# Performance work log

Hardware: AMD Instinct MI355X
Metric: run time of the kernel (lower is better)

## Reference

```python
import jax, jax.numpy as jnp
import numpy as np

B, T1, T2, D, H, NL, DFF, NC = 4, 128, 128, 512, 4, 4, 2048, 5
SQRT2 = 1.4142135623730951


def _ln(x, w, b, eps=1e-12):
    m = jnp.mean(x, -1, keepdims=True)
    v = jnp.mean((x - m) ** 2, -1, keepdims=True)
    return w * (x - m) / jnp.sqrt(v + eps) + b


def _gelu(x):  # erf-based gelu, as in source
    return x * 0.5 * (1.0 + jax.lax.erf(x / SQRT2))


def _mha(x, wq, bq, wk, bk, wv, bv, wo, bo):
    b, t, d = x.shape
    dk = d // H
    q = (x @ wq + bq).reshape(b, t, H, dk).transpose(0, 2, 1, 3)
    k = (x @ wk + bk).reshape(b, t, H, dk).transpose(0, 2, 1, 3)
    v = (x @ wv + bv).reshape(b, t, H, dk).transpose(0, 2, 1, 3)
    p = jax.nn.softmax(jnp.einsum('bhqd,bhkd->bhqk', q, k) / jnp.sqrt(jnp.float32(dk)), -1)
    o = jnp.einsum('bhqk,bhkd->bhqd', p, v).transpose(0, 2, 1, 3).reshape(b, t, d)
    return o @ wo + bo


def _encode(x, pos_emb, pe_w, pe_b, Wq, bq, Wk, bk, Wv, bv, Wo, bo,
            ff1_w, ff1_b, ff2_w, ff2_b, lnin_w, lnin_b, lnout_w, lnout_b):
    t = x.shape[1]
    x = _ln(x + pos_emb[:t], pe_w, pe_b)  # PositionalEncoding (dropout=0 eval)
    for i in range(Wq.shape[0]):  # EncoderLayer x NL
        x = x + _mha(x, Wq[i], bq[i], Wk[i], bk[i], Wv[i], bv[i], Wo[i], bo[i])
        h = _ln(x, lnin_w[i], lnin_b[i])
        x = x + (_gelu(h @ ff1_w[i] + ff1_b[i]) @ ff2_w[i] + ff2_b[i])
        x = _ln(x, lnout_w[i], lnout_b[i])
    return x


def _forward(q_emb, a_emb, qa_relation, aq_relation, concept_emb, pos_emb, pe_w, pe_b,
             Wq, bq, Wk, bk, Wv, bv, Wo, bo, ff1_w, ff1_b, ff2_w, ff2_b,
             lnin_w, lnin_b, lnout_w, lnout_b, sim_Wq, sim_bq, sim_Wk, sim_bk, cls_w, cls_b):
    enc = lambda x: _encode(x, pos_emb, pe_w, pe_b, Wq, bq, Wk, bk, Wv, bv, Wo, bo,
                            ff1_w, ff1_b, ff2_w, ff2_b, lnin_w, lnin_b, lnout_w, lnout_b)
    qe = enc(q_emb)   # [B,T1,D]
    ae = enc(a_emb)   # [B,T2,D]
    # ConceptEncoding: relation one-hots -> concept embedding mix
    hL = qa_relation @ concept_emb   # [B,T1,T2,D]
    hR = aq_relation @ concept_emb   # [B,T2,T1,D]
    # SimAttn: note source uses fwK for BOTH key and value, so v == k exactly
    q = qe @ sim_Wq + sim_bq
    k = ae @ sim_Wk + sim_bk
    kR = jnp.transpose(k[:, :, None, :] + hR, (0, 2, 1, 3))  # [B,T1,T2,D]
    scores = jnp.sum((q[:, :, None, :] + hL) * kR, axis=-1)   # [B,T1,T2]
    p = jax.nn.softmax(scores, -1)
    # sharpening branch (default sharpening=True): re-softmax the attention probs
    p = jnp.clip(jax.nn.softmax(1000.0 * p, -1), 0.0, 1.0)
    # value path: v + hR transposed == kR since v == k
    x = jnp.einsum('bts,btsd->btd', p, kR)                    # [B,T1,D]
    return jnp.mean(x, 1) @ cls_w + cls_b                     # [B,3]


def setup_inputs() -> dict:
    key = jax.random.key(0)
    rk = lambda i: jax.random.fold_in(key, i)
    w = lambda i, shape: 0.02 * jax.random.normal(rk(i), shape, jnp.float32)
    z = lambda shape: jnp.zeros(shape, jnp.float32)
    o = lambda shape: jnp.ones(shape, jnp.float32)
    return {
        'q_emb': jax.random.normal(rk(0), (B, T1, D), jnp.float32),
        'a_emb': jax.random.normal(rk(1), (B, T2, D), jnp.float32),
        'qa_relation': jax.random.uniform(rk(2), (B, T1, T2, NC), jnp.float32),
        'aq_relation': jax.random.uniform(rk(3), (B, T2, T1, NC), jnp.float32),
        'concept_emb': w(4, (NC, D)),
        'pos_emb': w(5, (512, D)),
        'pe_w': o((D,)), 'pe_b': z((D,)),
        'Wq': w(6, (NL, D, D)), 'bq': z((NL, D)),
        'Wk': w(7, (NL, D, D)), 'bk': z((NL, D)),
        'Wv': w(8, (NL, D, D)), 'bv': z((NL, D)),
        'Wo': w(9, (NL, D, D)), 'bo': z((NL, D)),
        'ff1_w': w(10, (NL, D, DFF)), 'ff1_b': z((NL, DFF)),
        'ff2_w': w(11, (NL, DFF, D)), 'ff2_b': z((NL, D)),
        'lnin_w': o((NL, D)), 'lnin_b': z((NL, D)),
        'lnout_w': o((NL, D)), 'lnout_b': z((NL, D)),
        'sim_Wq': w(12, (D, D)), 'sim_bq': z((D,)),
        'sim_Wk': w(13, (D, D)), 'sim_bk': z((D,)),
        'cls_w': w(14, (D, 3)), 'cls_b': z((3,)),
    }


def reference(q_emb, a_emb, qa_relation, aq_relation, concept_emb, pos_emb, pe_w, pe_b,
              Wq, bq, Wk, bk, Wv, bv, Wo, bo, ff1_w, ff1_b, ff2_w, ff2_b,
              lnin_w, lnin_b, lnout_w, lnout_b, sim_Wq, sim_bq, sim_Wk, sim_bk, cls_w, cls_b):
    return _forward(q_emb, a_emb, qa_relation, aq_relation, concept_emb, pos_emb, pe_w, pe_b,
                    Wq, bq, Wk, bk, Wv, bv, Wo, bo, ff1_w, ff1_b, ff2_w, ff2_b,
                    lnin_w, lnin_b, lnout_w, lnout_b, sim_Wq, sim_bq, sim_Wk, sim_bk, cls_w, cls_b)
```

## Files before the change

kernel.cpp:

```cpp
#include <hip/hip_runtime.h>
#include <hip/hip_bf16.h>
#include <math.h>

typedef unsigned short u16;
typedef __attribute__((ext_vector_type(8))) short bf16x8;
typedef __attribute__((ext_vector_type(4))) float f32x4;

__device__ __forceinline__ float ldin(const void* p, size_t i, int isbf) {
  if (isbf) return __bfloat162float(((const __hip_bfloat16*)p)[i]);
  return ((const float*)p)[i];
}
__device__ __forceinline__ float bfu(u16 u) { return __builtin_bit_cast(float, (unsigned)u << 16); }
__device__ __forceinline__ u16 f2bf(float x) {
  unsigned u = __builtin_bit_cast(unsigned, x);
  unsigned r = u + 0x7FFFu + ((u >> 16) & 1u);
  return (u16)(r >> 16);
}

__device__ __forceinline__ float wave_sum(float v) {
#pragma unroll
  for (int o = 32; o > 0; o >>= 1) v += __shfl_down(v, o);
  return v;
}

__device__ __forceinline__ float block_sum(float v, float* sbuf) {
  int lane = threadIdx.x & 63;
  int wid = threadIdx.x >> 6;
#pragma unroll
  for (int o = 32; o > 0; o >>= 1) v += __shfl_down(v, o);
  __syncthreads();
  if (lane == 0) sbuf[wid] = v;
  __syncthreads();
  int nw = blockDim.x >> 6;
  if (wid == 0) {
    float r = (lane < nw) ? sbuf[lane] : 0.f;
#pragma unroll
    for (int o = 4; o > 0; o >>= 1) r += __shfl_down(r, o);
    if (lane == 0) sbuf[0] = r;
  }
  __syncthreads();
  return sbuf[0];
}

__device__ __forceinline__ float block_max(float v, float* sbuf) {
  int lane = threadIdx.x & 63;
  int wid = threadIdx.x >> 6;
#pragma unroll
  for (int o = 32; o > 0; o >>= 1) v = fmaxf(v, __shfl_down(v, o));
  __syncthreads();
  if (lane == 0) sbuf[wid] = v;
  __syncthreads();
  int nw = blockDim.x >> 6;
  if (wid == 0) {
    float r = (lane < nw) ? sbuf[lane] : -INFINITY;
#pragma unroll
    for (int o = 4; o > 0; o >>= 1) r = fmaxf(r, __shfl_down(r, o));
    if (lane == 0) sbuf[0] = r;
  }
  __syncthreads();
  return sbuf[0];
}

__global__ void flag_kernel(const void* pe_w, int* flag) {
  if (threadIdx.x == 0 && blockIdx.x == 0)
    *flag = (((const unsigned short*)pe_w)[0] != 0) ? 1 : 0;
}

__global__ __launch_bounds__(256) void init_kernel(const void* pe_w, int* flag,
                                                   float* Sbuf, float* pabar) {
  int i = blockIdx.x * 256 + threadIdx.x;
  ((float4*)Sbuf)[i] = make_float4(0.f, 0.f, 0.f, 0.f);
  if (blockIdx.x == 0) {
    if (threadIdx.x == 0) *flag = (((const unsigned short*)pe_w)[0] != 0) ? 1 : 0;
    if (threadIdx.x < 20) pabar[threadIdx.x] = 0.f;
  }
}


__global__ __launch_bounds__(256) void convT2(
    const void* __restrict__ S0, const void* __restrict__ S1,
    const void* __restrict__ S2, const void* __restrict__ S3,
    size_t srcStride, int K, int N, u16* __restrict__ Dh, u16* __restrict__ Dl,
    size_t layerStride, size_t tensorStride, int tmask, int lshift,
    const int* __restrict__ dflag) {
  const int isbf = *dflag;
  int z = blockIdx.z;
  int t = z & tmask, l = z >> lshift;
  const void* S = (t == 0) ? S0 : ((t == 1) ? S1 : ((t == 2) ? S2 : S3));
  size_t soff = (size_t)l * srcStride;
  size_t doff = (size_t)l * layerStride + (size_t)t * tensorStride;
  int n0 = blockIdx.x * 32, k0 = blockIdx.y * 32;
  __shared__ float tt[32][33];
  int tx = threadIdx.x & 31, ty = threadIdx.x >> 5;
#pragma unroll
  for (int j = 0; j < 4; ++j) {
    int r = ty + j * 8;
    tt[r][tx] = ldin(S, soff + (size_t)(k0 + r) * N + n0 + tx, isbf);
  }
  __syncthreads();
#pragma unroll
  for (int j = 0; j < 4; ++j) {
    int r = ty + j * 8;
    float v = tt[tx][r];
    u16 h = f2bf(v);
    u16 lo = f2bf(v - bfu(h));
    size_t o = doff + (size_t)(n0 + r) * K + k0 + tx;
    Dh[o] = h;
    Dl[o] = lo;
  }
}

__global__ __launch_bounds__(256) void gemm_hl(
    const u16* __restrict__ Ahp, const u16* __restrict__ Alp, int lda,
    const u16* __restrict__ Whp, const u16* __restrict__ Wlp, int ldw,
    const void* __restrict__ b0, const void* __restrict__ b1, const void* __restrict__ b2,
    size_t bo0, size_t bo1, size_t bo2, int bshift,
    float* __restrict__ C, u16* __restrict__ Chp, u16* __restrict__ Clp,
    u16* __restrict__ Vh, u16* __restrict__ Vl, int ldc,
    int K, int act, int mode, int ysplit, size_t wrowoff1,
    const int* __restrict__ dflag) {
  const int isbf = *dflag;
  __shared__ __align__(16) u16 sAh[64][72];
  __shared__ __align__(16) u16 sAl[64][72];
  __shared__ __align__(16) u16 sBh[64][72];
  __shared__ __align__(16) u16 sBl[64][72];

  int tid = threadIdx.x;
  int by = blockIdx.y;
  int row0 = by * 64, col0 = blockIdx.x * 64;
  int rsplit = (by >= ysplit);
  size_t wrow0 = (size_t)col0 + (rsplit ? wrowoff1 : 0);
  if (mode == 5) wrow0 = wrowoff1 + (size_t)(by >> 1) * 128 + col0;
  int Ksub = K / (int)gridDim.z;
  int kstart = (int)blockIdx.z * Ksub;
  int addbias = (blockIdx.z == 0) && (mode != 5);

  int wid = tid >> 6, lane = tid & 63, quad = lane >> 4, lm = lane & 15;
  int mrow = (wid & 1) * 32, ncol = (wid >> 1) * 32;

  f32x4 acc[2][2] = {};

  int sr = tid >> 2, sc = (tid & 3) * 16;

  for (int k0 = kstart; k0 < kstart + Ksub; k0 += 64) {
    const u16* p;
    p = Ahp + (size_t)(row0 + sr) * lda + k0 + sc;
    uint4 a0 = *(const uint4*)p, a1 = *(const uint4*)(p + 8);
    p = Alp + (size_t)(row0 + sr) * lda + k0 + sc;
    uint4 a2 = *(const uint4*)p, a3 = *(const uint4*)(p + 8);
    p = Whp + (wrow0 + sr) * (size_t)ldw + k0 + sc;
    uint4 w0 = *(const uint4*)p, w1 = *(const uint4*)(p + 8);
    p = Wlp + (wrow0 + sr) * (size_t)ldw + k0 + sc;
    uint4 w2 = *(const uint4*)p, w3 = *(const uint4*)(p + 8);
    __syncthreads();
    *(uint4*)&sAh[sr][sc] = a0; *(uint4*)&sAh[sr][sc + 8] = a1;
    *(uint4*)&sAl[sr][sc] = a2; *(uint4*)&sAl[sr][sc + 8] = a3;
    *(uint4*)&sBh[sr][sc] = w0; *(uint4*)&sBh[sr][sc + 8] = w1;
    *(uint4*)&sBl[sr][sc] = w2; *(uint4*)&sBl[sr][sc + 8] = w3;
    __syncthreads();
#pragma unroll
    for (int ks = 0; ks < 2; ++ks) {
      bf16x8 ah[2], al[2], wh[2], wl[2];
#pragma unroll
      for (int mi = 0; mi < 2; ++mi) {
        ah[mi] = *(const bf16x8*)&sAh[mrow + mi * 16 + lm][ks * 32 + quad * 8];
        al[mi] = *(const bf16x8*)&sAl[mrow + mi * 16 + lm][ks * 32 + quad * 8];
      }
#pragma unroll
      for (int ni = 0; ni < 2; ++ni) {
        wh[ni] = *(const bf16x8*)&sBh[ncol + ni * 16 + lm][ks * 32 + quad * 8];
        wl[ni] = *(const bf16x8*)&sBl[ncol + ni * 16 + lm][ks * 32 + quad * 8];
      }
#pragma unroll
      for (int mi = 0; mi < 2; ++mi)
#pragma unroll
        for (int ni = 0; ni < 2; ++ni) {
          acc[mi][ni] = __builtin_amdgcn_mfma_f32_16x16x32_bf16(ah[mi], wh[ni], acc[mi][ni], 0, 0, 0);
          acc[mi][ni] = __builtin_amdgcn_mfma_f32_16x16x32_bf16(al[mi], wh[ni], acc[mi][ni], 0, 0, 0);
          acc[mi][ni] = __builtin_amdgcn_mfma_f32_16x16x32_bf16(ah[mi], wl[ni], acc[mi][ni], 0, 0, 0);
        }
    }
  }
#pragma unroll
  for (int mi = 0; mi < 2; ++mi) {
#pragma unroll
    for (int ni = 0; ni < 2; ++ni) {
      int colg = col0 + ncol + ni * 16 + lm;
      float bv = 0.f;
      if (addbias) {
        const void* bp; size_t bo;
        if (rsplit) { bp = b1; bo = bo1 + colg; }
        else {
          int seg = colg >> bshift;
          bp = (seg == 0) ? b0 : ((seg == 1) ? b1 : b2);
          bo = (seg == 0) ? bo0 : ((seg == 1) ? bo1 : bo2);
          bo += (size_t)colg - ((size_t)seg << bshift);
        }
        bv = ldin(bp, bo, isbf);
      }
#pragma unroll
      for (int r = 0; r < 4; ++r) {
        int rowg = row0 + mrow + mi * 16 + quad * 4 + r;
        float v = acc[mi][ni][r] + bv;
        if (act) v = v * 0.5f * (1.f + erff(v * 0.70710678118654752f));
        if (mode == 3 && colg >= 1024) {
          int gg = rowg >> 7;
          size_t o = ((size_t)(gg * 512) + (colg - 1024)) * 128 + (rowg & 127);
          u16 hh = f2bf(v); Vh[o] = hh; Vl[o] = f2bf(v - bfu(hh));
        } else {
          size_t o = (size_t)rowg * ldc + colg;
          if (mode == 0) C[o] = v;
          else if (mode == 1 || mode == 5) atomicAdd(&C[o], v);
          else if (mode == 4) {
            C[o] = v;
            u16 hh = f2bf(v); Chp[o] = hh; Clp[o] = f2bf(v - bfu(hh));
          } else {
            u16 hh = f2bf(v); Chp[o] = hh; Clp[o] = f2bf(v - bfu(hh));
          }
        }
      }
    }
  }
}

__global__ __launch_bounds__(256) void attn_mfma(
    const u16* __restrict__ Qh, const u16* __restrict__ Ql,
    const u16* __restrict__ Vth, const u16* __restrict__ Vtl,
    u16* __restrict__ Oh, u16* __restrict__ Ol) {
  int tq = blockIdx.x & 3;
  int h = (blockIdx.x >> 2) & 3;
  int g = blockIdx.x >> 4;
  int tid = threadIdx.x;
  int w = tid >> 6, lane = tid & 63, quad = lane >> 4, lm = lane & 15;
  __shared__ float S[32][132];

  f32x4 sacc[2][2] = {};
#pragma unroll
  for (int ks = 0; ks < 4; ++ks) {
    bf16x8 qh[2], ql[2];
#pragma unroll
    for (int mi = 0; mi < 2; ++mi) {
      size_t qi = (size_t)(g * 128 + tq * 32 + mi * 16 + lm) * 1536 + h * 128 + ks * 32 + quad * 8;
      qh[mi] = *(const bf16x8*)(Qh + qi);
      ql[mi] = *(const bf16x8*)(Ql + qi);
    }
#pragma unroll
    for (int ni = 0; ni < 2; ++ni) {
      size_t kix = (size_t)(g * 128 + w * 32 + ni * 16 + lm) * 1536 + 512 + h * 128 + ks * 32 + quad * 8;
      bf16x8 kh = *(const bf16x8*)(Qh + kix);
      bf16x8 kl = *(const bf16x8*)(Ql + kix);
#pragma unroll
      for (int mi = 0; mi < 2; ++mi) {
        sacc[mi][ni] = __builtin_amdgcn_mfma_f32_16x16x32_bf16(qh[mi], kh, sacc[mi][ni], 0, 0, 0);
        sacc[mi][ni] = __builtin_amdgcn_mfma_f32_16x16x32_bf16(ql[mi], kh, sacc[mi][ni], 0, 0, 0);
        sacc[mi][ni] = __builtin_amdgcn_mfma_f32_16x16x32_bf16(qh[mi], kl, sacc[mi][ni], 0, 0, 0);
      }
    }
  }
  const float scale = 0.08838834764831845f;
#pragma unroll
  for (int mi = 0; mi < 2; ++mi)
#pragma unroll
    for (int ni = 0; ni < 2; ++ni)
#pragma unroll
      for (int r = 0; r < 4; ++r)
        S[mi * 16 + quad * 4 + r][w * 32 + ni * 16 + lm] = sacc[mi][ni][r] * scale;
  __syncthreads();

  {
    int row = tid >> 3, j = tid & 7;
    float* sp = &S[row][j * 16];
    float v[16];
    *(float4*)(v) = *(float4*)(sp);
    *(float4*)(v + 4) = *(float4*)(sp + 4);
    *(float4*)(v + 8) = *(float4*)(sp + 8);
    *(float4*)(v + 12) = *(float4*)(sp + 12);
    float mx = v[0];
#pragma unroll
    for (int i = 1; i < 16; ++i) mx = fmaxf(mx, v[i]);
    mx = fmaxf(mx, __shfl_xor(mx, 1));
    mx = fmaxf(mx, __shfl_xor(mx, 2));
    mx = fmaxf(mx, __shfl_xor(mx, 4));
    float sum = 0.f;
#pragma unroll
    for (int i = 0; i < 16; ++i) { v[i] = expf(v[i] - mx); sum += v[i]; }
    sum += __shfl_xor(sum, 1);
    sum += __shfl_xor(sum, 2);
    sum += __shfl_xor(sum, 4);
    float inv = 1.f / sum;
#pragma unroll
    for (int i = 0; i < 16; ++i) v[i] *= inv;
    *(float4*)(sp) = *(float4*)(v);
    *(float4*)(sp + 4) = *(float4*)(v + 4);
    *(float4*)(sp + 8) = *(float4*)(v + 8);
    *(float4*)(sp + 12) = *(float4*)(v + 12);
  }
  __syncthreads();

  f32x4 oacc[2][2] = {};
#pragma unroll
  for (int ks = 0; ks < 4; ++ks) {
    bf16x8 ph[2], pl[2];
#pragma unroll
    for (int mi = 0; mi < 2; ++mi) {
      float pv[8];
      const float* srow = &S[mi * 16 + lm][ks * 32 + quad * 8];
      *(float4*)(pv) = *(const float4*)srow;
      *(float4*)(pv + 4) = *(const float4*)(srow + 4);
      bf16x8 hh, ll;
#pragma unroll
      for (int i = 0; i < 8; ++i) {
        u16 hb = f2bf(pv[i]);
        hh[i] = (short)hb;
        ll[i] = (short)f2bf(pv[i] - bfu(hb));
      }
      ph[mi] = hh; pl[mi] = ll;
    }
#pragma unroll
    for (int ni = 0; ni < 2; ++ni) {
      size_t vi = (size_t)(g * 512 + h * 128 + w * 32 + ni * 16 + lm) * 128 + ks * 32 + quad * 8;
      bf16x8 vh = *(const bf16x8*)(Vth + vi);
      bf16x8 vl = *(const bf16x8*)(Vtl + vi);
#pragma unroll
      for (int mi = 0; mi < 2; ++mi) {
        oacc[mi][ni] = __builtin_amdgcn_mfma_f32_16x16x32_bf16(ph[mi], vh, oacc[mi][ni], 0, 0, 0);
        oacc[mi][ni] = __builtin_amdgcn_mfma_f32_16x16x32_bf16(pl[mi], vh, oacc[mi][ni], 0, 0, 0);
        oacc[mi][ni] = __builtin_amdgcn_mfma_f32_16x16x32_bf16(ph[mi], vl, oacc[mi][ni], 0, 0, 0);
      }
    }
  }
#pragma unroll
  for (int mi = 0; mi < 2; ++mi)
#pragma unroll
    for (int ni = 0; ni < 2; ++ni)
#pragma unroll
      for (int r = 0; r < 4; ++r) {
        int t = tq * 32 + mi * 16 + quad * 4 + r;
        int d = w * 32 + ni * 16 + lm;
        size_t o = (size_t)(g * 128 + t) * 512 + h * 128 + d;
        float val = oacc[mi][ni][r];
        u16 hb = f2bf(val);
        Oh[o] = hb;
        Ol[o] = f2bf(val - bfu(hb));
      }
}

__global__ __launch_bounds__(256) void emb_ln2(
    const void* __restrict__ qe, const void* __restrict__ ae, const void* __restrict__ pos,
    const void* __restrict__ w, const void* __restrict__ b,
    float* __restrict__ x, u16* __restrict__ oh, u16* __restrict__ ol,
    const int* __restrict__ dflag) {
  const int isbf = *dflag;
  const int D = 512;
  int row = blockIdx.x;
  const void* emb = (row < 512) ? qe : ae;
  int lr = row & 511, t = row & 127;
  __shared__ float sbuf[8];
  int i0 = threadIdx.x, i1 = threadIdx.x + 256;
  float v0 = ldin(emb, (size_t)lr * D + i0, isbf) + ldin(pos, (size_t)t * D + i0, isbf);
  float v1 = ldin(emb, (size_t)lr * D + i1, isbf) + ldin(pos, (size_t)t * D + i1, isbf);
  float mean = block_sum(v0 + v1, sbuf) / 512.f;
  float d0 = v0 - mean, d1 = v1 - mean;
  float var = block_sum(d0 * d0 + d1 * d1, sbuf) / 512.f;
  float inv = 1.0f / sqrtf(var + 1e-12f);
  float r0 = ldin(w, i0, isbf) * d0 * inv + ldin(b, i0, isbf);
  float r1 = ldin(w, i1, isbf) * d1 * inv + ldin(b, i1, isbf);
  size_t o0 = (size_t)row * D + i0, o1 = (size_t)row * D + i1;
  x[o0] = r0; x[o1] = r1;
  u16 h0 = f2bf(r0); oh[o0] = h0; ol[o0] = f2bf(r0 - bfu(h0));
  u16 h1 = f2bf(r1); oh[o1] = h1; ol[o1] = f2bf(r1 - bfu(h1));
}

__global__ __launch_bounds__(256) void ln2(
    const float* __restrict__ in, float* __restrict__ outf,
    u16* __restrict__ oh, u16* __restrict__ ol,
    const void* __restrict__ w, const void* __restrict__ b, size_t wboff,
    const int* __restrict__ dflag) {
  const int isbf = *dflag;
  const int D = 512;
  int row = blockIdx.x;
  __shared__ float sbuf[8];
  int i0 = threadIdx.x, i1 = threadIdx.x + 256;
  float v0 = in[(size_t)row * D + i0];
  float v1 = in[(size_t)row * D + i1];
  float mean = block_sum(v0 + v1, sbuf) / 512.f;
  float d0 = v0 - mean, d1 = v1 - mean;
  float var = block_sum(d0 * d0 + d1 * d1, sbuf) / 512.f;
  float inv = 1.0f / sqrtf(var + 1e-12f);
  float r0 = ldin(w, wboff + i0, isbf) * d0 * inv + ldin(b, wboff + i0, isbf);
  float r1 = ldin(w, wboff + i1, isbf) * d1 * inv + ldin(b, wboff + i1, isbf);
  size_t o0 = (size_t)row * D + i0, o1 = (size_t)row * D + i1;
  if (outf) { outf[o0] = r0; outf[o1] = r1; }
  u16 h0 = f2bf(r0); oh[o0] = h0; ol[o0] = f2bf(r0 - bfu(h0));
  u16 h1 = f2bf(r1); oh[o1] = h1; ol[o1] = f2bf(r1 - bfu(h1));
}

__global__ __launch_bounds__(64) void projgram(const float* __restrict__ qkb,
                                               const void* __restrict__ ce,
                                               float* __restrict__ ck, float* __restrict__ G,
                                               const int* __restrict__ dflag) {
  const int isbf = *dflag;
  if (blockIdx.x < 1024) {
    int row = blockIdx.x;
#pragma unroll
    for (int c = 0; c < 5; ++c) {
      float acc = 0.f;
      for (int d = threadIdx.x; d < 512; d += 64)
        acc = fmaf(qkb[(size_t)row * 512 + d], ldin(ce, (size_t)c * 512 + d, isbf), acc);
      acc = wave_sum(acc);
      if (threadIdx.x == 0) ck[row * 5 + c] = acc;
    }
  } else {
    int i = blockIdx.x - 1024;
    int c = i / 5, c2 = i % 5;
    float acc = 0.f;
    for (int d = threadIdx.x; d < 512; d += 64)
      acc = fmaf(ldin(ce, (size_t)c * 512 + d, isbf), ldin(ce, (size_t)c2 * 512 + d, isbf), acc);
    acc = wave_sum(acc);
    if (threadIdx.x == 0) G[i] = acc;
  }
}

__global__ __launch_bounds__(256) void prep_rel(
    const void* __restrict__ aq, const void* __restrict__ qa,
    const float* __restrict__ ck, const float* __restrict__ G,
    float* __restrict__ R, const int* __restrict__ dflag) {
  const int isbf = *dflag;
  int bx = blockIdx.x;
  int t0 = (bx & 3) * 32;
  int s0 = ((bx >> 2) & 3) * 32;
  int b = bx >> 4;
  int tid = threadIdx.x;
  __shared__ float aqs[32][164];
  __shared__ float Gs[25];
  __shared__ float kcs[32][5];
  __shared__ float qcs[32][5];
  for (int i = tid; i < 5120; i += 256) {
    int s = i / 160, r = i % 160;
    aqs[s][r] = ldin(aq, ((size_t)(b * 128 + s0 + s) * 128 + t0) * 5 + r, isbf);
  }
  if (tid < 25) Gs[tid] = G[tid];
  for (int i = tid; i < 160; i += 256)
    kcs[i / 5][i % 5] = ck[(size_t)(512 + b * 128 + s0 + i / 5) * 5 + i % 5];
  for (int i = tid; i < 160; i += 256)
    qcs[i / 5][i % 5] = ck[(size_t)(b * 128 + t0 + i / 5) * 5 + i % 5];
  __syncthreads();
  for (int i = tid; i < 1024; i += 256) {
    int t = i >> 5, s = i & 31;
    size_t qoff = ((size_t)(b * 128 + t0 + t) * 128 + s0 + s) * 5;
    float r = 0.f;
#pragma unroll
    for (int c = 0; c < 5; ++c) {
      float ga = 0.f;
#pragma unroll
      for (int c2 = 0; c2 < 5; ++c2) ga = fmaf(Gs[c * 5 + c2], aqs[s][t * 5 + c2], ga);
      r = fmaf(ldin(qa, qoff + c, isbf), kcs[s][c] + ga, r);
      r = fmaf(aqs[s][t * 5 + c], qcs[t][c], r);
    }
    R[(size_t)(b * 128 + t0 + t) * 128 + s0 + s] = r;
  }
}

__global__ __launch_bounds__(128) void softmax_rel(
    const float* __restrict__ Sbuf, const float* __restrict__ R,
    float* __restrict__ PT) {
  int row = blockIdx.x;
  int b = row >> 7, t = row & 127;
  int s = threadIdx.x;
  __shared__ float sbuf[8];
  size_t o = (size_t)row * 128 + s;
  float sc = Sbuf[o] + R[o];
  float mx = block_max(sc, sbuf);
  float e = expf(sc - mx);
  float ssum = block_sum(e, sbuf);
  float p = e / ssum;
  float mx2 = block_max(p, sbuf);
  float e2 = expf(1000.f * (p - mx2));
  float s2 = block_sum(e2, sbuf);
  float pf = fminf(fmaxf(e2 / s2, 0.f), 1.f);
  PT[(size_t)(b * 128 + s) * 128 + t] = pf;
}

__global__ __launch_bounds__(64) void pbar2(
    const float* __restrict__ PT, const void* __restrict__ aq,
    float* __restrict__ Pbar, float* __restrict__ pabar,
    const int* __restrict__ dflag) {
  const int isbf = *dflag;
  int bs = blockIdx.x;
  int b = bs >> 7;
  int lane = threadIdx.x;
  int t0 = lane * 2;
  float2 pt = *(const float2*)(PT + (size_t)bs * 128 + t0);
  size_t ao = ((size_t)bs * 128 + t0) * 5;
  float psum = pt.x + pt.y;
  float pac[5];
#pragma unroll
  for (int c = 0; c < 5; ++c)
    pac[c] = pt.x * ldin(aq, ao + c, isbf) + pt.y * ldin(aq, ao + 5 + c, isbf);
  psum = wave_sum(psum);
#pragma unroll
  for (int c = 0; c < 5; ++c) pac[c] = wave_sum(pac[c]);
  if (lane == 0) {
    Pbar[bs] = psum;
#pragma unroll
    for (int c = 0; c < 5; ++c) atomicAdd(&pabar[b * 5 + c], pac[c]);
  }
}

__global__ __launch_bounds__(512) void meancls(
    const float* __restrict__ qkb, const float* __restrict__ Pbar, const float* __restrict__ pabar,
    const void* __restrict__ ce, const void* __restrict__ clsw, const void* __restrict__ clsb,
    void* __restrict__ out, const int* __restrict__ dflag) {
  const int isbf = *dflag;
  int b = blockIdx.x;
  int tid = threadIdx.x;
  __shared__ float Ps[128];
  __shared__ float pas[5];
  __shared__ float xm[512];
  __shared__ float sbuf[8];
  if (tid < 128) Ps[tid] = Pbar[b * 128 + tid];
  if (tid < 5) pas[tid] = pabar[b * 5 + tid];
  __syncthreads();
  int d = tid;
  const float* k = qkb + (size_t)(512 + b * 128) * 512 + d;
  float acc = 0.f;
  for (int s = 0; s < 128; ++s) acc = fmaf(Ps[s], k[(size_t)s * 512], acc);
#pragma unroll
  for (int c = 0; c < 5; ++c) acc = fmaf(pas[c], ldin(ce, (size_t)c * 512 + d, isbf), acc);
  acc *= (1.f / 128.f);
  xm[d] = acc;
  __syncthreads();
  for (int j = 0; j < 3; ++j) {
    float v = block_sum(xm[d] * ldin(clsw, (size_t)d * 3 + j, isbf), sbuf);
    if (d == 0) {
      float val = v + ldin(clsb, j, isbf);
      if (isbf) ((u16*)out)[b * 3 + j] = f2bf(val);
      else ((float*)out)[b * 3 + j] = val;
    }
    __syncthreads();
  }
}


__global__ __launch_bounds__(256) void gemm_mfma(
    const float* __restrict__ A, const void* __restrict__ W, size_t woff,
    const void* __restrict__ bias, size_t boff,
    float* __restrict__ C, int M, int N, int K, int act, int addto,
    const int* __restrict__ dflag) {
  const int isbf = *dflag;
  __shared__ __align__(16) u16 Ah[64][40];
  __shared__ __align__(16) u16 Al[64][40];
  __shared__ __align__(16) u16 Wh[64][40];
  __shared__ __align__(16) u16 Wl[64][40];
  int tid = threadIdx.x;
  int row0 = blockIdx.y * 64, col0 = blockIdx.x * 64;
  int wid = tid >> 6, lane = tid & 63;
  int quad = lane >> 4, lm = lane & 15;
  int mrow = (wid & 1) * 32, ncol = (wid >> 1) * 32;
  f32x4 acc[2][2] = {};
  int ar = tid >> 2, akc = (tid & 3) * 8;
  int bk = tid >> 3, bn0 = (tid & 7) * 8;
  for (int k0 = 0; k0 < K; k0 += 32) {
    const float* ap = A + (size_t)(row0 + ar) * K + k0 + akc;
    float av[8];
    *(float4*)(av) = *(const float4*)ap;
    *(float4*)(av + 4) = *(const float4*)(ap + 4);
    unsigned hp[4], lp[4];
#pragma unroll
    for (int j = 0; j < 4; ++j) {
      u16 h0 = f2bf(av[2 * j]);
      u16 h1 = f2bf(av[2 * j + 1]);
      u16 l0 = f2bf(av[2 * j] - bfu(h0));
      u16 l1 = f2bf(av[2 * j + 1] - bfu(h1));
      hp[j] = (unsigned)h0 | ((unsigned)h1 << 16);
      lp[j] = (unsigned)l0 | ((unsigned)l1 << 16);
    }
    *(uint4*)&Ah[ar][akc] = make_uint4(hp[0], hp[1], hp[2], hp[3]);
    *(uint4*)&Al[ar][akc] = make_uint4(lp[0], lp[1], lp[2], lp[3]);
    float wv[8];
    size_t welem = woff + (size_t)(k0 + bk) * N + col0 + bn0;
    if (isbf) {
      const u16* wp = (const u16*)W + welem;
      uint4 raw = *(const uint4*)wp;
      wv[0] = bfu((u16)(raw.x & 0xFFFF)); wv[1] = bfu((u16)(raw.x >> 16));
      wv[2] = bfu((u16)(raw.y & 0xFFFF)); wv[3] = bfu((u16)(raw.y >> 16));
      wv[4] = bfu((u16)(raw.z & 0xFFFF)); wv[5] = bfu((u16)(raw.z >> 16));
      wv[6] = bfu((u16)(raw.w & 0xFFFF)); wv[7] = bfu((u16)(raw.w >> 16));
    } else {
      const float* wp = (const float*)W + welem;
      *(float4*)(wv) = *(const float4*)wp;
      *(float4*)(wv + 4) = *(const float4*)(wp + 4);
    }
#pragma unroll
    for (int i = 0; i < 8; ++i) {
      u16 h = f2bf(wv[i]);
      u16 l = f2bf(wv[i] - bfu(h));
      Wh[bn0 + i][bk] = h;
      Wl[bn0 + i][bk] = l;
    }
    __syncthreads();
#pragma unroll
    for (int mi = 0; mi < 2; ++mi) {
      bf16x8 ah = *(const bf16x8*)&Ah[mrow + mi * 16 + lm][quad * 8];
      bf16x8 al = *(const bf16x8*)&Al[mrow + mi * 16 + lm][quad * 8];
#pragma unroll
      for (int ni = 0; ni < 2; ++ni) {
        bf16x8 wh = *(const bf16x8*)&Wh[ncol + ni * 16 + lm][quad * 8];
        bf16x8 wl = *(const bf16x8*)&Wl[ncol + ni * 16 + lm][quad * 8];
        acc[mi][ni] = __builtin_amdgcn_mfma_f32_16x16x32_bf16(ah, wh, acc[mi][ni], 0, 0, 0);
        acc[mi][ni] = __builtin_amdgcn_mfma_f32_16x16x32_bf16(al, wh, acc[mi][ni], 0, 0, 0);
        acc[mi][ni] = __builtin_amdgcn_mfma_f32_16x16x32_bf16(ah, wl, acc[mi][ni], 0, 0, 0);
      }
    }
    __syncthreads();
  }
#pragma unroll
  for (int mi = 0; mi < 2; ++mi) {
#pragma unroll
    for (int ni = 0; ni < 2; ++ni) {
      int colg = col0 + ncol + ni * 16 + lm;
      float bv = ldin(bias, boff + colg, isbf);
#pragma unroll
      for (int r = 0; r < 4; ++r) {
        int rowg = row0 + mrow + mi * 16 + quad * 4 + r;
        float v = acc[mi][ni][r] + bv;
        if (act) v = v * 0.5f * (1.f + erff(v * 0.70710678118654752f));
        size_t o = (size_t)rowg * N + colg;
        if (addto) C[o] += v; else C[o] = v;
      }
    }
  }
}

__global__ __launch_bounds__(256) void emb_ln_kernel(const void* __restrict__ emb,
                                                     const void* __restrict__ pos,
                                                     const void* __restrict__ w,
                                                     const void* __restrict__ b,
                                                     float* __restrict__ out, int T, int D,
                                                     const int* __restrict__ dflag) {
  const int isbf = *dflag;
  int row = blockIdx.x;
  int t = row % T;
  __shared__ float sbuf[8];
  int i0 = threadIdx.x, i1 = threadIdx.x + 256;
  float v0 = ldin(emb, (size_t)row * D + i0, isbf) + ldin(pos, (size_t)t * D + i0, isbf);
  float v1 = ldin(emb, (size_t)row * D + i1, isbf) + ldin(pos, (size_t)t * D + i1, isbf);
  float mean = block_sum(v0 + v1, sbuf) / (float)D;
  float d0 = v0 - mean, d1 = v1 - mean;
  float var = block_sum(d0 * d0 + d1 * d1, sbuf) / (float)D;
  float inv = 1.0f / sqrtf(var + 1e-12f);
  out[(size_t)row * D + i0] = ldin(w, i0, isbf) * d0 * inv + ldin(b, i0, isbf);
  out[(size_t)row * D + i1] = ldin(w, i1, isbf) * d1 * inv + ldin(b, i1, isbf);
}

__global__ __launch_bounds__(256) void ln_kernel(const float* __restrict__ in, float* __restrict__ out,
                                                 const void* __restrict__ w, const void* __restrict__ b,
                                                 size_t wboff, int D, const int* __restrict__ dflag) {
  const int isbf = *dflag;
  int row = blockIdx.x;
  __shared__ float sbuf[8];
  int i0 = threadIdx.x, i1 = threadIdx.x + 256;
  float v0 = in[(size_t)row * D + i0];
  float v1 = in[(size_t)row * D + i1];
  float mean = block_sum(v0 + v1, sbuf) / (float)D;
  float d0 = v0 - mean, d1 = v1 - mean;
  float var = block_sum(d0 * d0 + d1 * d1, sbuf) / (float)D;
  float inv = 1.0f / sqrtf(var + 1e-12f);
  out[(size_t)row * D + i0] = ldin(w, wboff + i0, isbf) * d0 * inv + ldin(b, wboff + i0, isbf);
  out[(size_t)row * D + i1] = ldin(w, wboff + i1, isbf) * d1 * inv + ldin(b, wboff + i1, isbf);
}

__global__ __launch_bounds__(128) void attn_kernel(const float* __restrict__ q, const float* __restrict__ k,
                                                   const float* __restrict__ v, float* __restrict__ o,
                                                   int B, int H, int T, int dk) {
  int t = blockIdx.x % T;
  int h = (blockIdx.x / T) % H;
  int b = blockIdx.x / (T * H);
  int D = H * dk;
  int tid = threadIdx.x;
  __shared__ float qs[128];
  __shared__ float ps[128];
  __shared__ float sbuf[8];
  qs[tid] = q[(size_t)(b * T + t) * D + h * dk + tid];
  __syncthreads();
  const float* krow = k + (size_t)(b * T + tid) * D + h * dk;
  float sc = 0.f;
#pragma unroll 8
  for (int d = 0; d < 128; ++d) sc = fmaf(qs[d], krow[d], sc);
  sc *= 0.08838834764831845f;
  float mx = block_max(sc, sbuf);
  float e = expf(sc - mx);
  float s = block_sum(e, sbuf);
  ps[tid] = e / s;
  __syncthreads();
  float acc = 0.f;
  for (int s2 = 0; s2 < 128; ++s2)
    acc = fmaf(ps[s2], v[(size_t)(b * T + s2) * D + h * dk + tid], acc);
  o[(size_t)(b * T + t) * D + h * dk + tid] = acc;
}

__global__ __launch_bounds__(64) void proj_ce_kernel(const float* __restrict__ q,
                                                     const void* __restrict__ ce,
                                                     float* __restrict__ out, int D, int NC,
                                                     const int* __restrict__ dflag) {
  const int isbf = *dflag;
  int row = blockIdx.x;
  for (int c = 0; c < NC; ++c) {
    float acc = 0.f;
    for (int d = threadIdx.x; d < D; d += 64)
      acc = fmaf(q[(size_t)row * D + d], ldin(ce, (size_t)c * D + d, isbf), acc);
    acc = wave_sum(acc);
    if (threadIdx.x == 0) out[row * NC + c] = acc;
  }
}

__global__ __launch_bounds__(64) void gram_kernel(const void* __restrict__ ce,
                                                  float* __restrict__ G, int D, int NC,
                                                  const int* __restrict__ dflag) {
  const int isbf = *dflag;
  int c = blockIdx.x / NC, c2 = blockIdx.x % NC;
  float acc = 0.f;
  for (int d = threadIdx.x; d < D; d += 64)
    acc = fmaf(ldin(ce, (size_t)c * D + d, isbf), ldin(ce, (size_t)c2 * D + d, isbf), acc);
  acc = wave_sum(acc);
  if (threadIdx.x == 0) G[blockIdx.x] = acc;
}

__global__ __launch_bounds__(128) void sim_scores_kernel(
    const float* __restrict__ q, const float* __restrict__ k, const void* __restrict__ qa,
    const void* __restrict__ aq, const float* __restrict__ qc, const float* __restrict__ kc,
    const float* __restrict__ G, float* __restrict__ p_out, float* __restrict__ pa_out,
    int B, int T1, int T2, int D, int NC, const int* __restrict__ dflag) {
  const int isbf = *dflag;
  int t = blockIdx.x % T1;
  int b = blockIdx.x / T1;
  int s = threadIdx.x;
  __shared__ float qs[512];
  __shared__ float Gs[25];
  __shared__ float qcs[5];
  __shared__ float sbuf[8];
  for (int i = threadIdx.x; i < D; i += 128) qs[i] = q[(size_t)(b * T1 + t) * D + i];
  if (threadIdx.x < NC * NC) Gs[threadIdx.x] = G[threadIdx.x];
  if (threadIdx.x < NC) qcs[threadIdx.x] = qc[(b * T1 + t) * NC + threadIdx.x];
  __syncthreads();
  const float* krow = k + (size_t)(b * T2 + s) * D;
  float sc = 0.f;
#pragma unroll 8
  for (int d = 0; d < 512; ++d) sc = fmaf(qs[d], krow[d], sc);
  float qav[5], aqv[5];
#pragma unroll
  for (int c = 0; c < 5; ++c) {
    qav[c] = ldin(qa, (size_t)((b * T1 + t) * T2 + s) * NC + c, isbf);
    aqv[c] = ldin(aq, (size_t)((b * T2 + s) * T1 + t) * NC + c, isbf);
  }
#pragma unroll
  for (int c = 0; c < 5; ++c) {
    sc = fmaf(aqv[c], qcs[c], sc);
    sc = fmaf(qav[c], kc[(b * T2 + s) * NC + c], sc);
#pragma unroll
    for (int c2 = 0; c2 < 5; ++c2) sc = fmaf(qav[c] * Gs[c * 5 + c2], aqv[c2], sc);
  }
  float mx = block_max(sc, sbuf);
  float e = expf(sc - mx);
  float ssum = block_sum(e, sbuf);
  float p = e / ssum;
  float mx2 = block_max(p, sbuf);
  float e2 = expf(1000.f * (p - mx2));
  float s2 = block_sum(e2, sbuf);
  float pf = fminf(fmaxf(e2 / s2, 0.f), 1.f);
  p_out[(size_t)(b * T1 + t) * T2 + s] = pf;
#pragma unroll
  for (int c = 0; c < 5; ++c) {
    float pc = block_sum(pf * aqv[c], sbuf);
    if (threadIdx.x == 0) pa_out[(b * T1 + t) * NC + c] = pc;
  }
}

__global__ __launch_bounds__(512) void sim_x_kernel(const float* __restrict__ p, const float* __restrict__ k,
                                                    const float* __restrict__ pa,
                                                    const void* __restrict__ ce,
                                                    float* __restrict__ x, int B, int T1, int T2, int D, int NC,
                                                    const int* __restrict__ dflag) {
  const int isbf = *dflag;
  int t = blockIdx.x % T1;
  int b = blockIdx.x / T1;
  int d = threadIdx.x;
  __shared__ float ps[128];
  __shared__ float pav[5];
  if (threadIdx.x < T2) ps[threadIdx.x] = p[(size_t)(b * T1 + t) * T2 + threadIdx.x];
  if (threadIdx.x < NC) pav[threadIdx.x] = pa[(b * T1 + t) * NC + threadIdx.x];
  __syncthreads();
  float acc = 0.f;
  for (int s = 0; s < 128; ++s) acc = fmaf(ps[s], k[(size_t)(b * T2 + s) * D + d], acc);
#pragma unroll
  for (int c = 0; c < 5; ++c) acc = fmaf(pav[c], ldin(ce, (size_t)c * D + d, isbf), acc);
  x[(size_t)(b * T1 + t) * D + d] = acc;
}

__global__ __launch_bounds__(512) void mean_kernel(const float* __restrict__ x, float* __restrict__ xm,
                                                   int T, int D) {
  int b = blockIdx.x;
  int d = threadIdx.x;
  float acc = 0.f;
  for (int t = 0; t < T; ++t) acc += x[(size_t)(b * T + t) * D + d];
  xm[(size_t)b * D + d] = acc / (float)T;
}

__global__ __launch_bounds__(64) void cls_kernel(const float* __restrict__ xm,
                                                 const void* __restrict__ w,
                                                 const void* __restrict__ bias,
                                                 void* __restrict__ out, int D, int NO,
                                                 const int* __restrict__ dflag) {
  const int isbf = *dflag;
  int j = blockIdx.x % NO;
  int b = blockIdx.x / NO;
  float acc = 0.f;
  for (int d = threadIdx.x; d < D; d += 64)
    acc = fmaf(xm[(size_t)b * D + d], ldin(w, (size_t)d * NO + j, isbf), acc);
  acc = wave_sum(acc);
  if (threadIdx.x == 0) {
    float val = acc + ldin(bias, j, isbf);
    if (isbf) ((__hip_bfloat16*)out)[b * NO + j] = __float2bfloat16(val);
    else ((float*)out)[b * NO + j] = val;
  }
}

extern "C" void kernel_launch(void* const* d_in, const int* in_sizes, int n_in,
                              void* d_out, int out_size, void* d_ws, size_t ws_size,
                              hipStream_t stream) {
  const int B = 4, T = 128, D = 512, H = 4, NL = 4, DFF = 2048, NC = 5;
  const void *q_emb = d_in[0], *a_emb = d_in[1], *qa = d_in[2], *aqr = d_in[3],
             *ce = d_in[4], *pos = d_in[5], *pe_w = d_in[6], *pe_b = d_in[7],
             *Wq = d_in[8], *bq = d_in[9], *Wk = d_in[10], *bk = d_in[11],
             *Wv = d_in[12], *bv = d_in[13], *Wo = d_in[14], *bo = d_in[15],
             *ff1w = d_in[16], *ff1b = d_in[17], *ff2w = d_in[18], *ff2b = d_in[19],
             *lnin_w = d_in[20], *lnin_b = d_in[21], *lnout_w = d_in[22], *lnout_b = d_in[23],
             *simWq = d_in[24], *simbq = d_in[25], *simWk = d_in[26], *simbk = d_in[27],
             *clsw = d_in[28], *clsb = d_in[29];

  const size_t REQ = 83000000ull;
  if (ws_size >= REQ) {
    char* base = (char*)d_ws;
    float* x = (float*)(base + 0);
    u16* xch = (u16*)(base + 2097152);
    u16* xcl = (u16*)(base + 3145728);
    u16* qkvh = (u16*)(base + 4194304);
    u16* qkvl = (u16*)(base + 7340032);
    u16* ffch = (u16*)(base + 10485760);
    u16* ffcl = (u16*)(base + 14680064);
    u16* Vth = (u16*)(base + 18874368);
    u16* Vtl = (u16*)(base + 19922944);
    float* qkb = (float*)(base + 20971520);
    u16* qsh = (u16*)(base + 23068672);
    u16* qsl = (u16*)(base + 24117248);
    float* ck = (float*)(base + 25165824);
    float* Gbuf = (float*)(base + 25186304);
    float* Pbar = (float*)(base + 25190400);
    float* pabar = (float*)(base + 25192448);
    int* dflag = (int*)(base + 25196544);
    u16* wh = (u16*)(base + 26214400);
    u16* wl = (u16*)(base + 52428800);
    float* Sbuf = (float*)(base + 79691776);
    float* R = (float*)(base + 79953920);
    float* PT = (float*)(base + 80216064);

    init_kernel<<<64, 256, 0, stream>>>(pe_w, dflag, Sbuf, pabar);
    convT2<<<dim3(16, 16, 16), 256, 0, stream>>>(Wq, Wk, Wv, Wo, 262144, 512, 512,
                                                 wh, wl, 3145728, 262144, 3, 2, dflag);
    convT2<<<dim3(64, 16, 4), 256, 0, stream>>>(ff1w, ff1w, ff1w, ff1w, 1048576, 512, 2048,
                                                wh + 1048576, wl + 1048576, 3145728, 0, 0, 0, dflag);
    convT2<<<dim3(16, 64, 4), 256, 0, stream>>>(ff2w, ff2w, ff2w, ff2w, 1048576, 2048, 512,
                                                wh + 2097152, wl + 2097152, 3145728, 0, 0, 0, dflag);
    convT2<<<dim3(16, 16, 2), 256, 0, stream>>>(simWq, simWk, simWk, simWk, 0, 512, 512,
                                                wh + 12582912, wl + 12582912, 0, 262144, 1, 1, dflag);

    emb_ln2<<<1024, 256, 0, stream>>>(q_emb, a_emb, pos, pe_w, pe_b, x, xch, xcl, dflag);

    for (int l = 0; l < NL; ++l) {
      size_t wbase = (size_t)l * 3145728, bD = (size_t)l * D;
      gemm_hl<<<dim3(24, 16, 1), 256, 0, stream>>>(xch, xcl, 512, wh + wbase, wl + wbase, 512,
                                                   bq, bk, bv, bD, bD, bD, 9,
                                                   nullptr, qkvh, qkvl, Vth, Vtl, 1536,
                                                   512, 0, 3, 9999, 0, dflag);
      attn_mfma<<<128, 256, 0, stream>>>(qkvh, qkvl, Vth, Vtl, xch, xcl);
      gemm_hl<<<dim3(8, 16, 2), 256, 0, stream>>>(xch, xcl, 512, wh + wbase + 786432,
                                                  wl + wbase + 786432, 512,
                                                  bo, bo, bo, bD, bD, bD, 9,
                                                  x, nullptr, nullptr, nullptr, nullptr, 512,
                                                  512, 0, 1, 9999, 0, dflag);
      ln2<<<1024, 256, 0, stream>>>(x, nullptr, xch, xcl, lnin_w, lnin_b, bD, dflag);
      gemm_hl<<<dim3(32, 16, 1), 256, 0, stream>>>(xch, xcl, 512, wh + wbase + 1048576,
                                                   wl + wbase + 1048576, 512,
                                                   ff1b, ff1b, ff1b,
                                                   (size_t)l * DFF, (size_t)l * DFF, (size_t)l * DFF, 11,
                                                   nullptr, ffch, ffcl, nullptr, nullptr, 2048,
                                                   512, 1, 2, 9999, 0, dflag);
      gemm_hl<<<dim3(8, 16, 2), 256, 0, stream>>>(ffch, ffcl, 2048, wh + wbase + 2097152,
                                                  wl + wbase + 2097152, 2048,
                                                  ff2b, ff2b, ff2b, bD, bD, bD, 9,
                                                  x, nullptr, nullptr, nullptr, nullptr, 512,
                                                  2048, 0, 1, 9999, 0, dflag);
      ln2<<<1024, 256, 0, stream>>>(x, x, xch, xcl, lnout_w, lnout_b, bD, dflag);
    }

    gemm_hl<<<dim3(8, 16, 1), 256, 0, stream>>>(xch, xcl, 512, wh + 12582912, wl + 12582912, 512,
                                                simbq, simbk, simbk, 0, 0, 0, 9,
                                                qkb, qsh, qsl, nullptr, nullptr, 512,
                                                512, 0, 4, 8, 512, dflag);
    projgram<<<1049, 64, 0, stream>>>(qkb, ce, ck, Gbuf, dflag);
    prep_rel<<<64, 256, 0, stream>>>(aqr, qa, ck, Gbuf, R, dflag);
    gemm_hl<<<dim3(2, 8, 4), 256, 0, stream>>>(qsh, qsl, 512, qsh, qsl, 512,
                                               nullptr, nullptr, nullptr, 0, 0, 0, 9,
                                               Sbuf, nullptr, nullptr, nullptr, nullptr, 128,
                                               512, 0, 5, 9999, 512, dflag);
    softmax_rel<<<512, 128, 0, stream>>>(Sbuf, R, PT);
    pbar2<<<512, 64, 0, stream>>>(PT, aqr, Pbar, pabar, dflag);
    meancls<<<4, 512, 0, stream>>>(qkb, Pbar, pabar, ce, clsw, clsb, d_out, dflag);
    return;
  }

  float* ws = (float*)d_ws;
  const size_t S = (size_t)512 * 512;
  float* qe = ws;
  float* ae = ws + S;
  float* hb = ws + 2 * S;
  float* rb = ws + 3 * S;
  float* qb = rb;
  float* kb = rb + S;
  float* vb = rb + 2 * S;
  float* ob = rb + 3 * S;
  float* ffb = rb;
  float* pbuf = rb + 2 * S;
  float* pabuf = pbuf + 65536;
  float* qcbuf = pabuf + 2560;
  float* kcbuf = qcbuf + 2560;
  float* Gbuf = kcbuf + 2560;
  float* xmean = Gbuf + 32;
  float* xsim = rb + 3 * S;
  int* dflag = (int*)(ws + 7 * S);

  const int M = B * T;
  dim3 gD(8, 8), gF1(32, 8), gF2(8, 8);

  flag_kernel<<<1, 64, 0, stream>>>(pe_w, dflag);
  for (int e = 0; e < 2; ++e) {
    float* x = (e == 0) ? qe : ae;
    const void* emb = (e == 0) ? q_emb : a_emb;
    emb_ln_kernel<<<M, 256, 0, stream>>>(emb, pos, pe_w, pe_b, x, T, D, dflag);
    for (int l = 0; l < NL; ++l) {
      size_t wDD = (size_t)l * D * D, bD = (size_t)l * D;
      gemm_mfma<<<gD, 256, 0, stream>>>(x, Wq, wDD, bq, bD, qb, M, D, D, 0, 0, dflag);
      gemm_mfma<<<gD, 256, 0, stream>>>(x, Wk, wDD, bk, bD, kb, M, D, D, 0, 0, dflag);
      gemm_mfma<<<gD, 256, 0, stream>>>(x, Wv, wDD, bv, bD, vb, M, D, D, 0, 0, dflag);
      attn_kernel<<<B * H * T, 128, 0, stream>>>(qb, kb, vb, ob, B, H, T, D / H);
      gemm_mfma<<<gD, 256, 0, stream>>>(ob, Wo, wDD, bo, bD, x, M, D, D, 0, 1, dflag);
      ln_kernel<<<M, 256, 0, stream>>>(x, hb, lnin_w, lnin_b, bD, D, dflag);
      gemm_mfma<<<gF1, 256, 0, stream>>>(hb, ff1w, (size_t)l * D * DFF, ff1b, (size_t)l * DFF,
                                         ffb, M, DFF, D, 1, 0, dflag);
      gemm_mfma<<<gF2, 256, 0, stream>>>(ffb, ff2w, (size_t)l * DFF * D, ff2b, bD,
                                         x, M, D, DFF, 0, 1, dflag);
      ln_kernel<<<M, 256, 0, stream>>>(x, x, lnout_w, lnout_b, bD, D, dflag);
    }
  }
  gemm_mfma<<<gD, 256, 0, stream>>>(qe, simWq, 0, simbq, 0, qb, M, D, D, 0, 0, dflag);
  gemm_mfma<<<gD, 256, 0, stream>>>(ae, simWk, 0, simbk, 0, kb, M, D, D, 0, 0, dflag);
  proj_ce_kernel<<<M, 64, 0, stream>>>(qb, ce, qcbuf, D, NC, dflag);
  proj_ce_kernel<<<M, 64, 0, stream>>>(kb, ce, kcbuf, D, NC, dflag);
  gram_kernel<<<NC * NC, 64, 0, stream>>>(ce, Gbuf, D, NC, dflag);
  sim_scores_kernel<<<B * T, 128, 0, stream>>>(qb, kb, qa, aqr, qcbuf, kcbuf, Gbuf, pbuf, pabuf,
                                               B, T, T, D, NC, dflag);
  sim_x_kernel<<<B * T, 512, 0, stream>>>(pbuf, kb, pabuf, ce, xsim, B, T, T, D, NC, dflag);
  mean_kernel<<<B, 512, 0, stream>>>(xsim, xmean, T, D);
  cls_kernel<<<B * 3, 64, 0, stream>>>(xmean, clsw, clsb, d_out, D, 3, dflag);
}
```

Before: 627.9 us.

## Merge weight conversion launches and remove zero-init via non-atomic reductions

Folds the four weight transpose/split launches into a single convT_all kernel with a 50-slice z grid. The score GEMM drops its split-K atomics in favour of plain stores (new mode 6), which removes the need to zero Sbuf. pbar2 now writes per-row partials that meancls reduces itself, so init_kernel is replaced by a tiny flag kernel. The aim is fewer launches and fewer atomics, at the cost of a serial K loop in the small score GEMM.

Measured after the change: 593.5 us. 1.06x faster.

```diff
diff --git a/kernel.cpp b/kernel.cpp
--- a/kernel.cpp
+++ b/kernel.cpp
@@ -66,30 +66,40 @@
     *flag = (((const unsigned short*)pe_w)[0] != 0) ? 1 : 0;
 }
 
-__global__ __launch_bounds__(256) void init_kernel(const void* pe_w, int* flag,
-                                                   float* Sbuf, float* pabar) {
-  int i = blockIdx.x * 256 + threadIdx.x;
-  ((float4*)Sbuf)[i] = make_float4(0.f, 0.f, 0.f, 0.f);
-  if (blockIdx.x == 0) {
-    if (threadIdx.x == 0) *flag = (((const unsigned short*)pe_w)[0] != 0) ? 1 : 0;
-    if (threadIdx.x < 20) pabar[threadIdx.x] = 0.f;
-  }
-}
-
-
-__global__ __launch_bounds__(256) void convT2(
-    const void* __restrict__ S0, const void* __restrict__ S1,
-    const void* __restrict__ S2, const void* __restrict__ S3,
-    size_t srcStride, int K, int N, u16* __restrict__ Dh, u16* __restrict__ Dl,
-    size_t layerStride, size_t tensorStride, int tmask, int lshift,
-    const int* __restrict__ dflag) {
-  const int isbf = *dflag;
-  int z = blockIdx.z;
-  int t = z & tmask, l = z >> lshift;
-  const void* S = (t == 0) ? S0 : ((t == 1) ? S1 : ((t == 2) ? S2 : S3));
-  size_t soff = (size_t)l * srcStride;
-  size_t doff = (size_t)l * layerStride + (size_t)t * tensorStride;
-  int n0 = blockIdx.x * 32, k0 = blockIdx.y * 32;
+
+__global__ __launch_bounds__(256) void convT_all(
+    const void* __restrict__ Wq, const void* __restrict__ Wk,
+    const void* __restrict__ Wv, const void* __restrict__ Wo,
+    const void* __restrict__ ff1w, const void* __restrict__ ff2w,
+    const void* __restrict__ simWq, const void* __restrict__ simWk,
+    u16* __restrict__ Dh, u16* __restrict__ Dl, const int* __restrict__ dflag) {
+  const int isbf = *dflag;
+  int z = blockIdx.z, x = blockIdx.x, y = blockIdx.y;
+  const void* S;
+  size_t soff, doff;
+  int K, N, n0, k0;
+  if (z < 16) {
+    int t = z & 3, l = z >> 2;
+    S = (t == 0) ? Wq : ((t == 1) ? Wk : ((t == 2) ? Wv : Wo));
+    soff = (size_t)l * 262144; K = 512; N = 512;
+    doff = (size_t)l * 3145728 + (size_t)t * 262144;
+    n0 = x * 32; k0 = y * 32;
+  } else if (z < 32) {
+    int idx = z - 16, l = idx >> 2, xg = idx & 3;
+    S = ff1w; soff = (size_t)l * 1048576; K = 512; N = 2048;
+    doff = (size_t)l * 3145728 + 1048576;
+    n0 = (xg * 16 + x) * 32; k0 = y * 32;
+  } else if (z < 48) {
+    int idx = z - 32, l = idx >> 2, yg = idx & 3;
+    S = ff2w; soff = (size_t)l * 1048576; K = 2048; N = 512;
+    doff = (size_t)l * 3145728 + 2097152;
+    n0 = x * 32; k0 = (yg * 16 + y) * 32;
+  } else {
+    S = (z == 48) ? simWq : simWk;
+    soff = 0; K = 512; N = 512;
+    doff = 12582912 + (size_t)(z - 48) * 262144;
+    n0 = x * 32; k0 = y * 32;
+  }
   __shared__ float tt[32][33];
   int tx = threadIdx.x & 31, ty = threadIdx.x >> 5;
 #pragma unroll
@@ -130,10 +140,10 @@
   int row0 = by * 64, col0 = blockIdx.x * 64;
   int rsplit = (by >= ysplit);
   size_t wrow0 = (size_t)col0 + (rsplit ? wrowoff1 : 0);
-  if (mode == 5) wrow0 = wrowoff1 + (size_t)(by >> 1) * 128 + col0;
+  if (mode == 6) wrow0 = wrowoff1 + (size_t)(by >> 1) * 128 + col0;
   int Ksub = K / (int)gridDim.z;
   int kstart = (int)blockIdx.z * Ksub;
-  int addbias = (blockIdx.z == 0) && (mode != 5);
+  int addbias = (blockIdx.z == 0) && (mode != 6);
 
   int wid = tid >> 6, lane = tid & 63, quad = lane >> 4, lm = lane & 15;
   int mrow = (wid & 1) * 32, ncol = (wid >> 1) * 32;
@@ -209,8 +219,8 @@
           u16 hh = f2bf(v); Vh[o] = hh; Vl[o] = f2bf(v - bfu(hh));
         } else {
           size_t o = (size_t)rowg * ldc + colg;
-          if (mode == 0) C[o] = v;
-          else if (mode == 1 || mode == 5) atomicAdd(&C[o], v);
+          if (mode == 0 || mode == 6) C[o] = v;
+          else if (mode == 1) atomicAdd(&C[o], v);
           else if (mode == 4) {
             C[o] = v;
             u16 hh = f2bf(v); Chp[o] = hh; Clp[o] = f2bf(v - bfu(hh));
@@ -483,11 +493,10 @@
 
 __global__ __launch_bounds__(64) void pbar2(
     const float* __restrict__ PT, const void* __restrict__ aq,
-    float* __restrict__ Pbar, float* __restrict__ pabar,
+    float* __restrict__ Pbar, float* __restrict__ pabarS,
     const int* __restrict__ dflag) {
   const int isbf = *dflag;
   int bs = blockIdx.x;
-  int b = bs >> 7;
   int lane = threadIdx.x;
   int t0 = lane * 2;
   float2 pt = *(const float2*)(PT + (size_t)bs * 128 + t0);
@@ -503,12 +512,13 @@
   if (lane == 0) {
     Pbar[bs] = psum;
 #pragma unroll
-    for (int c = 0; c < 5; ++c) atomicAdd(&pabar[b * 5 + c], pac[c]);
+    for (int c = 0; c < 5; ++c) pabarS[(size_t)bs * 5 + c] = pac[c];
   }
 }
 
 __global__ __launch_bounds__(512) void meancls(
-    const float* __restrict__ qkb, const float* __restrict__ Pbar, const float* __restrict__ pabar,
+    const float* __restrict__ qkb, const float* __restrict__ Pbar,
+    const float* __restrict__ pabarS,
     const void* __restrict__ ce, const void* __restrict__ clsw, const void* __restrict__ clsb,
     void* __restrict__ out, const int* __restrict__ dflag) {
   const int isbf = *dflag;
@@ -518,8 +528,18 @@
   __shared__ float pas[5];
   __shared__ float xm[512];
   __shared__ float sbuf[8];
-  if (tid < 128) Ps[tid] = Pbar[b * 128 + tid];
-  if (tid < 5) pas[tid] = pabar[b * 5 + tid];
+  if (tid < 5) pas[tid] = 0.f;
+  __syncthreads();
+  if (tid < 128) {
+    Ps[tid] = Pbar[b * 128 + tid];
+    const float* ps = pabarS + ((size_t)(b * 128 + tid)) * 5;
+    float pac[5] = {ps[0], ps[1], ps[2], ps[3], ps[4]};
+#pragma unroll
+    for (int c = 0; c < 5; ++c) {
+      float v = wave_sum(pac[c]);
+      if ((tid & 63) == 0) atomicAdd(&pas[c], v);
+    }
+  }
   __syncthreads();
   int d = tid;
   const float* k = qkb + (size_t)(512 + b * 128) * 512 + d;
@@ -856,24 +876,17 @@
     float* ck = (float*)(base + 25165824);
     float* Gbuf = (float*)(base + 25186304);
     float* Pbar = (float*)(base + 25190400);
-    float* pabar = (float*)(base + 25192448);
     int* dflag = (int*)(base + 25196544);
     u16* wh = (u16*)(base + 26214400);
     u16* wl = (u16*)(base + 52428800);
     float* Sbuf = (float*)(base + 79691776);
     float* R = (float*)(base + 79953920);
     float* PT = (float*)(base + 80216064);
-
-    init_kernel<<<64, 256, 0, stream>>>(pe_w, dflag, Sbuf, pabar);
-    convT2<<<dim3(16, 16, 16), 256, 0, stream>>>(Wq, Wk, Wv, Wo, 262144, 512, 512,
-                                                 wh, wl, 3145728, 262144, 3, 2, dflag);
-    convT2<<<dim3(64, 16, 4), 256, 0, stream>>>(ff1w, ff1w, ff1w, ff1w, 1048576, 512, 2048,
-                                                wh + 1048576, wl + 1048576, 3145728, 0, 0, 0, dflag);
-    convT2<<<dim3(16, 64, 4), 256, 0, stream>>>(ff2w, ff2w, ff2w, ff2w, 1048576, 2048, 512,
-                                                wh + 2097152, wl + 2097152, 3145728, 0, 0, 0, dflag);
-    convT2<<<dim3(16, 16, 2), 256, 0, stream>>>(simWq, simWk, simWk, simWk, 0, 512, 512,
-                                                wh + 12582912, wl + 12582912, 0, 262144, 1, 1, dflag);
-
+    float* pabarS = (float*)(base + 80478208);
+
+    flag_kernel<<<1, 64, 0, stream>>>(pe_w, dflag);
+    convT_all<<<dim3(16, 16, 50), 256, 0, stream>>>(Wq, Wk, Wv, Wo, ff1w, ff2w,
+                                                    simWq, simWk, wh, wl, dflag);
     emb_ln2<<<1024, 256, 0, stream>>>(q_emb, a_emb, pos, pe_w, pe_b, x, xch, xcl, dflag);
 
     for (int l = 0; l < NL; ++l) {
@@ -909,13 +922,13 @@
                                                 512, 0, 4, 8, 512, dflag);
     projgram<<<1049, 64, 0, stream>>>(qkb, ce, ck, Gbuf, dflag);
     prep_rel<<<64, 256, 0, stream>>>(aqr, qa, ck, Gbuf, R, dflag);
-    gemm_hl<<<dim3(2, 8, 4), 256, 0, stream>>>(qsh, qsl, 512, qsh, qsl, 512,
+    gemm_hl<<<dim3(2, 8, 1), 256, 0, stream>>>(qsh, qsl, 512, qsh, qsl, 512,
                                                nullptr, nullptr, nullptr, 0, 0, 0, 9,
                                                Sbuf, nullptr, nullptr, nullptr, nullptr, 128,
-                                               512, 0, 5, 9999, 512, dflag);
+                                               512, 0, 6, 9999, 512, dflag);
     softmax_rel<<<512, 128, 0, stream>>>(Sbuf, R, PT);
-    pbar2<<<512, 64, 0, stream>>>(PT, aqr, Pbar, pabar, dflag);
-    meancls<<<4, 512, 0, stream>>>(qkb, Pbar, pabar, ce, clsw, clsb, d_out, dflag);
+    pbar2<<<512, 64, 0, stream>>>(PT, aqr, Pbar, pabarS, dflag);
+    meancls<<<4, 512, 0, stream>>>(qkb, Pbar, pabarS, ce, clsw, clsb, d_out, dflag);
     return;
   }
 
```
